# Optimization experiments

Measured on AMD Instinct MI355X. Metric: run time of the kernel, lower is better.

Reference implementation:

```python
import jax, jax.numpy as jnp
import numpy as np

H, D, KV, S, PAST, BS, NB = 32, 128, 8, 128, 8064, 128, 128
T = PAST + S          # total context = 8192
NBLK = T // BS        # logical blocks used = 64
NEG = jnp.float32(-1e30)


def setup_inputs() -> dict:
    key = jax.random.key(0)
    ks = jax.random.split(key, 6)
    q = jax.random.normal(ks[0], (1, H, S, D), jnp.float32)
    k = jax.random.normal(ks[1], (1, KV, S, D), jnp.float32)
    v = jax.random.normal(ks[2], (1, KV, S, D), jnp.float32)
    pk = jax.random.normal(ks[3], (NB, KV, BS, D), jnp.float32)
    pv = jax.random.normal(ks[4], (NB, KV, BS, D), jnp.float32)
    # block table: 64 logical blocks mapped to distinct physical blocks (paged indirection)
    bt = jax.random.permutation(ks[5], NB)[:NBLK].astype(jnp.int32)
    return dict(
        query_state=q, key_state=k, value_state=v,
        attn_mask=jnp.ones((1,), jnp.float32),  # unused: causal prefill path (use_attention_mask=False)
        past_key_state=pk, past_value_state=pv,
        seq_position=PAST,
        scale=jnp.float32(1.0 / np.sqrt(D)),
        block_tables=bt, block_size=BS,
    )


def reference(query_state, key_state, value_state, attn_mask,
              past_key_state, past_value_state, seq_position, scale,
              block_tables, block_size):
    # phase == 'prefill', use_attention_mask=False -> paged_causal_attn_prefill
    kvh = past_key_state.shape[1]
    s_new = query_state.shape[2]
    total = seq_position + s_new  # static python int

    # --- append new K/V into the paged cache at positions [seq_position, total) ---
    pos_new = seq_position + jnp.arange(s_new)
    blk = block_tables[pos_new // block_size]
    off = pos_new % block_size
    k_new = jnp.transpose(key_state[0], (1, 0, 2))    # [S, KV, D]
    v_new = jnp.transpose(value_state[0], (1, 0, 2))
    kc = past_key_state.at[blk, :, off, :].set(k_new)
    vc = past_value_state.at[blk, :, off, :].set(v_new)

    # --- gather the full context [0, total) through the block table ---
    pos = jnp.arange(total)
    blk_a = block_tables[pos // block_size]
    off_a = pos % block_size
    K = kc[blk_a, :, off_a, :]   # [T, KV, D]
    V = vc[blk_a, :, off_a, :]

    # --- grouped-query causal attention ---
    g = query_state.shape[1] // kvh
    q = query_state.reshape(kvh, g, s_new, -1)                 # [KV, G, S, D]
    scores = jnp.einsum('kgsd,tkd->kgst', q, K) * scale        # [KV, G, S, T]
    causal = pos[None, :] <= (seq_position + jnp.arange(s_new))[:, None]  # [S, T]
    scores = jnp.where(causal[None, None], scores, NEG)
    probs = jax.nn.softmax(scores, axis=-1)
    out = jnp.einsum('kgst,tkd->kgsd', probs, V)               # [KV, G, S, D]

    h = kvh * g
    out = out.reshape(1, h, s_new, -1)                         # [1, H, S, D]
    out = jnp.transpose(out, (0, 2, 1, 3)).reshape(1, s_new, h * out.shape[-1])
    return out
```

## Files before the change

### kernel.cpp

```cpp
#include <hip/hip_runtime.h>
#include <hip/hip_bf16.h>


typedef unsigned short u16;
typedef unsigned int u32;
typedef __bf16 bf16x8 __attribute__((ext_vector_type(8)));
typedef float f32x16 __attribute__((ext_vector_type(16)));
typedef float f32x4 __attribute__((ext_vector_type(4)));
typedef u32 u32x4 __attribute__((ext_vector_type(4)));
typedef u32 u32x2 __attribute__((ext_vector_type(2)));
typedef int i32x2 __attribute__((ext_vector_type(2)));

#define NHEAD 32
#define DH 128
#define NKV 8
#define SQ 128
#define PAST_T 8064
#define TOTAL_T 8192
#define BK 64
#define KSTR 136
#define VSTR 66
#define WSPP (16384 + 256)
#define MSUB 17.3123405f

__device__ __forceinline__ u32 pk2f(float lo, float hi) {
  union {
    __hip_bfloat162 b;
    u32 u;
  } cv;
  cv.b = __float22bfloat162_rn(make_float2(lo, hi));
  return cv.u;
}

template <int NPART>
__global__ __launch_bounds__(512, 1) void flash_part(
    const float* __restrict__ q, const float* __restrict__ knew,
    const float* __restrict__ vnew, const float* __restrict__ pk,
    const float* __restrict__ pv, const int* __restrict__ btab,
    const float* __restrict__ scp, float* __restrict__ ws) {
  constexpr int CHUNK = TOTAL_T / NPART;
  constexpr int NITER = CHUNK / BK;
  __shared__ __attribute__((aligned(16))) u16 k_s[2 * BK * KSTR];
  __shared__ __attribute__((aligned(16))) u16 vt_s[2 * DH * VSTR];
  __shared__ int bt_s[64];

  const int bid = blockIdx.x;
  const int kv = bid & 7;
  const int t = bid >> 3;
  const int p = t % NPART;
  const int gp = t / NPART;

  const int tid = threadIdx.x;
  const int wid = tid >> 6;
  const int lane = tid & 63;
  const int g2 = wid & 1;
  const int w = wid >> 1;
  const int h = kv * 4 + gp * 2 + g2;
  const int l31 = lane & 31, grp = lane >> 5;
  const int pstart = p * CHUNK;

  if (tid < 64) bt_s[tid] = btab[tid];
  const float qs = scp[0] * 1.44269504f;

  u32x4 qf[8];
  {
    const float* qp = q + ((size_t)(h * SQ + w * 32 + l31)) * DH;
#pragma unroll
    for (int st = 0; st < 8; ++st) {
      const f32x4 a = *(const f32x4*)(qp + st * 16 + grp * 8);
      const f32x4 b = *(const f32x4*)(qp + st * 16 + grp * 8 + 4);
      u32x4 f;
      f[0] = pk2f(a[0] * qs, a[1] * qs);
      f[1] = pk2f(a[2] * qs, a[3] * qs);
      f[2] = pk2f(b[0] * qs, b[1] * qs);
      f[3] = pk2f(b[2] * qs, b[3] * qs);
      qf[st] = f;
    }
  }

  f32x16 oacc[4];
#pragma unroll
  for (int i = 0; i < 4; ++i)
#pragma unroll
    for (int rr = 0; rr < 16; ++rr) oacc[i][rr] = 0.0f;
  float l_acc = 0.0f;

  __syncthreads();

  f32x4 kr0, kr1, kr2, kr3, v0, v1, v2, v3;
  const int kc4 = (tid & 31) * 4;
  const int ktrow = tid >> 5;
  const int va4 = (tid & 31) * 4;
  const int vtp = tid >> 5;

  auto load_tile = [&](int it) {
    const int t0 = pstart + it * BK;
    const float *sk, *sv;
    if (t0 < PAST_T) {
      const size_t boff =
          (((size_t)bt_s[t0 >> 7] * NKV + kv) * 128 + (t0 & 127)) * (size_t)DH;
      sk = pk + boff;
      sv = pv + boff;
    } else {
      const size_t noff = ((size_t)kv * SQ + (t0 - PAST_T)) * (size_t)DH;
      sk = knew + noff;
      sv = vnew + noff;
    }
    kr0 = *(const f32x4*)(sk + (size_t)(ktrow + 0) * DH + kc4);
    kr1 = *(const f32x4*)(sk + (size_t)(ktrow + 16) * DH + kc4);
    kr2 = *(const f32x4*)(sk + (size_t)(ktrow + 32) * DH + kc4);
    kr3 = *(const f32x4*)(sk + (size_t)(ktrow + 48) * DH + kc4);
    v0 = *(const f32x4*)(sv + (size_t)(2 * vtp) * DH + va4);
    v1 = *(const f32x4*)(sv + (size_t)(2 * vtp + 1) * DH + va4);
    v2 = *(const f32x4*)(sv + (size_t)(2 * vtp + 32) * DH + va4);
    v3 = *(const f32x4*)(sv + (size_t)(2 * vtp + 33) * DH + va4);
  };
  auto store_tile = [&](int buf) {
    u16* ks = k_s + buf * (BK * KSTR);
    u16* vs = vt_s + buf * (DH * VSTR);
    {
      u32x2 pw;
      pw[0] = pk2f(kr0[0], kr0[1]);
      pw[1] = pk2f(kr0[2], kr0[3]);
      *(u32x2*)&ks[(ktrow + 0) * KSTR + kc4] = pw;
    }
    {
      u32x2 pw;
      pw[0] = pk2f(kr1[0], kr1[1]);
      pw[1] = pk2f(kr1[2], kr1[3]);
      *(u32x2*)&ks[(ktrow + 16) * KSTR + kc4] = pw;
    }
    {
      u32x2 pw;
      pw[0] = pk2f(kr2[0], kr2[1]);
      pw[1] = pk2f(kr2[2], kr2[3]);
      *(u32x2*)&ks[(ktrow + 32) * KSTR + kc4] = pw;
    }
    {
      u32x2 pw;
      pw[0] = pk2f(kr3[0], kr3[1]);
      pw[1] = pk2f(kr3[2], kr3[3]);
      *(u32x2*)&ks[(ktrow + 48) * KSTR + kc4] = pw;
    }
#pragma unroll
    for (int j = 0; j < 4; ++j) {
      *(u32*)&vs[(va4 + j) * VSTR + 2 * vtp] = pk2f(v0[j], v1[j]);
      *(u32*)&vs[(va4 + j) * VSTR + 2 * vtp + 32] = pk2f(v2[j], v3[j]);
    }
  };

  load_tile(0);
  store_tile(0);
  __syncthreads();

  for (int it = 0; it < NITER; ++it) {
    const int buf = it & 1;
    if (it + 1 < NITER) load_tile(it + 1);

    const u16* ks = k_s + buf * (BK * KSTR);
    const u16* vs = vt_s + buf * (DH * VSTR);
    const int t0 = pstart + it * BK;
    const int qcol = w * 32 + l31;

    f32x16 sacc0, sacc1;
#pragma unroll
    for (int rr = 0; rr < 16; ++rr) sacc0[rr] = 0.0f;
#pragma unroll
    for (int rr = 0; rr < 16; ++rr) sacc1[rr] = 0.0f;
#pragma unroll
    for (int st = 0; st < 8; ++st) {
      const u32x4 kf0 = *(const u32x4*)&ks[l31 * KSTR + st * 16 + grp * 8];
      sacc0 = __builtin_amdgcn_mfma_f32_32x32x16_bf16(
          __builtin_bit_cast(bf16x8, kf0), __builtin_bit_cast(bf16x8, qf[st]),
          sacc0, 0, 0, 0);
      const u32x4 kf1 =
          *(const u32x4*)&ks[(l31 + 32) * KSTR + st * 16 + grp * 8];
      sacc1 = __builtin_amdgcn_mfma_f32_32x32x16_bf16(
          __builtin_bit_cast(bf16x8, kf1), __builtin_bit_cast(bf16x8, qf[st]),
          sacc1, 0, 0, 0);
    }

#pragma unroll
    for (int ts = 0; ts < 2; ++ts) {
      const f32x16& sacc = ts ? sacc1 : sacc0;
      const int tb = t0 + ts * 32;

      float pr[16];
      if (tb > PAST_T - 32) {
#pragma unroll
        for (int rr = 0; rr < 16; ++rr) {
          const int trow = (rr & 3) + 8 * (rr >> 2) + 4 * grp;
          const float e = exp2f(sacc[rr] - MSUB);
          pr[rr] = ((tb + trow - PAST_T) > qcol) ? 0.0f : e;
        }
      } else {
#pragma unroll
        for (int rr = 0; rr < 16; ++rr) pr[rr] = exp2f(sacc[rr] - MSUB);
      }
      float rs = 0.0f;
#pragma unroll
      for (int rr = 0; rr < 16; ++rr) rs += pr[rr];
      l_acc += rs;

      u32 pkk[8];
#pragma unroll
      for (int j = 0; j < 8; ++j) pkk[j] = pk2f(pr[2 * j], pr[2 * j + 1]);

      u32x4 pf1, pf2;
#if __has_builtin(__builtin_amdgcn_permlane32_swap)
      {
        const i32x2 s02 = __builtin_amdgcn_permlane32_swap(
            (int)pkk[0], (int)pkk[2], false, false);
        const i32x2 s13 = __builtin_amdgcn_permlane32_swap(
            (int)pkk[1], (int)pkk[3], false, false);
        const i32x2 s46 = __builtin_amdgcn_permlane32_swap(
            (int)pkk[4], (int)pkk[6], false, false);
        const i32x2 s57 = __builtin_amdgcn_permlane32_swap(
            (int)pkk[5], (int)pkk[7], false, false);
        pf1[0] = (u32)s02[0];
        pf1[1] = (u32)s13[0];
        pf1[2] = (u32)s02[1];
        pf1[3] = (u32)s13[1];
        pf2[0] = (u32)s46[0];
        pf2[1] = (u32)s57[0];
        pf2[2] = (u32)s46[1];
        pf2[3] = (u32)s57[1];
      }
#else
      {
        u32 xch[8];
#pragma unroll
        for (int j = 0; j < 8; ++j)
          xch[j] = (u32)__shfl_xor((int)pkk[j], 32, 64);
        pf1[0] = grp ? xch[2] : pkk[0];
        pf1[1] = grp ? xch[3] : pkk[1];
        pf1[2] = grp ? pkk[2] : xch[0];
        pf1[3] = grp ? pkk[3] : xch[1];
        pf2[0] = grp ? xch[6] : pkk[4];
        pf2[1] = grp ? xch[7] : pkk[5];
        pf2[2] = grp ? pkk[6] : xch[4];
        pf2[3] = grp ? pkk[7] : xch[5];
      }
#endif

#pragma unroll
      for (int dt = 0; dt < 4; ++dt) {
        const int dd = dt * 32 + l31;
        const u16* vp = &vs[dd * VSTR + ts * 32 + grp * 8];
        u32x4 av;
        av[0] = *(const u32*)(vp + 0);
        av[1] = *(const u32*)(vp + 2);
        av[2] = *(const u32*)(vp + 4);
        av[3] = *(const u32*)(vp + 6);
        oacc[dt] = __builtin_amdgcn_mfma_f32_32x32x16_bf16(
            __builtin_bit_cast(bf16x8, av), __builtin_bit_cast(bf16x8, pf1),
            oacc[dt], 0, 0, 0);
        const u16* vq = vp + 16;
        u32x4 bv;
        bv[0] = *(const u32*)(vq + 0);
        bv[1] = *(const u32*)(vq + 2);
        bv[2] = *(const u32*)(vq + 4);
        bv[3] = *(const u32*)(vq + 6);
        oacc[dt] = __builtin_amdgcn_mfma_f32_32x32x16_bf16(
            __builtin_bit_cast(bf16x8, bv), __builtin_bit_cast(bf16x8, pf2),
            oacc[dt], 0, 0, 0);
      }
    }

    if (it + 1 < NITER) store_tile(buf ^ 1);
    __syncthreads();
  }

  float* wsp = ws + (size_t)(h * NPART + p) * WSPP;
#pragma unroll
  for (int dt = 0; dt < 4; ++dt)
#pragma unroll
    for (int rr = 0; rr < 16; ++rr) {
      const int dd = dt * 32 + (rr & 3) + 8 * (rr >> 2) + 4 * grp;
      wsp[dd * 128 + w * 32 + l31] = oacc[dt][rr];
    }
  const float l_tot = l_acc + __shfl_xor(l_acc, 32, 64);
  if (grp == 0) wsp[16384 + w * 32 + l31] = l_tot;
}

template <int NPART>
__global__ __launch_bounds__(256, 2) void combine_out(
    const float* __restrict__ ws, float* __restrict__ out) {
  __shared__ float rden_s[128];
  __shared__ float tr_s[128 * 9];

  const int dblk = blockIdx.x;
  const int h = blockIdx.y;
  const int tid = threadIdx.x;
  const float* base = ws + (size_t)h * NPART * WSPP;

  if (tid < 128) {
    float denom = 0.0f;
#pragma unroll
    for (int pp = 0; pp < NPART; ++pp)
      denom += base[(size_t)pp * WSPP + 16384 + tid];
    rden_s[tid] = 1.0f / denom;
  }
  __syncthreads();

  const int sq = tid & 31, dr = tid >> 5;
  {
    const int d = dblk * 8 + dr;
    float a[4] = {0.0f, 0.0f, 0.0f, 0.0f};
#pragma unroll
    for (int pp = 0; pp < NPART; ++pp) {
      const f32x4 o = *(const f32x4*)&base[(size_t)pp * WSPP + d * 128 + sq * 4];
#pragma unroll
      for (int j = 0; j < 4; ++j) a[j] += o[j];
    }
#pragma unroll
    for (int j = 0; j < 4; ++j)
      tr_s[(sq * 4 + j) * 9 + dr] = a[j] * rden_s[sq * 4 + j];
  }
  __syncthreads();

  {
    const int s = tid >> 1, dl0 = (tid & 1) * 4;
    f32x4 o;
#pragma unroll
    for (int j = 0; j < 4; ++j) o[j] = tr_s[s * 9 + dl0 + j];
    *(f32x4*)(out + (size_t)s * (NHEAD * DH) + h * DH + dblk * 8 + dl0) = o;
  }
}

extern "C" void kernel_launch(void* const* d_in, const int* in_sizes, int n_in,
                              void* d_out, int out_size, void* d_ws,
                              size_t ws_size, hipStream_t stream) {
  const float* q = (const float*)d_in[0];
  const float* knew = (const float*)d_in[1];
  const float* vnew = (const float*)d_in[2];
  const float* pk = (const float*)d_in[4];
  const float* pv = (const float*)d_in[5];
  const float* scp = (const float*)d_in[7];
  const int* btab = (const int*)d_in[8];
  float* ws = (float*)d_ws;
  float* out = (float*)d_out;

  const size_t need16 = (size_t)NHEAD * 16 * WSPP * sizeof(float);
  const size_t need8 = (size_t)NHEAD * 8 * WSPP * sizeof(float);
  if (ws_size >= need16) {
    flash_part<16><<<dim3(8 * 2 * 16), 512, 0, stream>>>(q, knew, vnew, pk, pv,
                                                         btab, scp, ws);
    combine_out<16><<<dim3(16, NHEAD), 256, 0, stream>>>(ws, out);
  } else if (ws_size >= need8) {
    flash_part<8><<<dim3(8 * 2 * 8), 512, 0, stream>>>(q, knew, vnew, pk, pv,
                                                       btab, scp, ws);
    combine_out<8><<<dim3(16, NHEAD), 256, 0, stream>>>(ws, out);
  }
}
```

Measured before the change: 170.2 us.

## Pre-swizzle V tile into MFMA fragment layout and simplify combine kernel

V tiles are now loaded as scalar columns per thread and stored to shared memory already packed in the MFMA operand-fragment order, so the PV inner loop reads each operand with one 128-bit LDS load instead of four 32-bit loads. This trades coalesced vector global loads of V for strided scalar loads (still coalesced across lanes along D). The combine kernel drops its shared-memory transpose and writes float2 outputs directly, using twice as many blocks with fewer columns each.

Measured after the change: 171.2 us. About the same (+0.6%).

```diff
diff --git a/kernel.cpp b/kernel.cpp
--- a/kernel.cpp
+++ b/kernel.cpp
@@ -19,7 +19,7 @@
 #define TOTAL_T 8192
 #define BK 64
 #define KSTR 136
-#define VSTR 66
+#define VT_SZ 8192
 #define WSPP (16384 + 256)
 #define MSUB 17.3123405f
 
@@ -41,7 +41,7 @@
   constexpr int CHUNK = TOTAL_T / NPART;
   constexpr int NITER = CHUNK / BK;
   __shared__ __attribute__((aligned(16))) u16 k_s[2 * BK * KSTR];
-  __shared__ __attribute__((aligned(16))) u16 vt_s[2 * DH * VSTR];
+  __shared__ __attribute__((aligned(16))) u16 vt_s[2 * VT_SZ];
   __shared__ int bt_s[64];
 
   const int bid = blockIdx.x;
@@ -87,11 +87,17 @@
 
   __syncthreads();
 
-  f32x4 kr0, kr1, kr2, kr3, v0, v1, v2, v3;
+  f32x4 kr0, kr1, kr2, kr3;
+  float va[8], vb[8];
   const int kc4 = (tid & 31) * 4;
   const int ktrow = tid >> 5;
-  const int va4 = (tid & 31) * 4;
-  const int vtp = tid >> 5;
+  const int vd = tid & 127;
+  const int tb8a = tid >> 7;
+  const int vofA =
+      ((((vd >> 5) * 4 + (tb8a >> 1)) * 2 + (tb8a & 1)) * 32 + (vd & 31)) * 8;
+  const int vofB =
+      ((((vd >> 5) * 4 + ((tb8a + 4) >> 1)) * 2 + ((tb8a + 4) & 1)) * 32 +
+       (vd & 31)) * 8;
 
   auto load_tile = [&](int it) {
     const int t0 = pstart + it * BK;
@@ -110,14 +116,16 @@
     kr1 = *(const f32x4*)(sk + (size_t)(ktrow + 16) * DH + kc4);
     kr2 = *(const f32x4*)(sk + (size_t)(ktrow + 32) * DH + kc4);
     kr3 = *(const f32x4*)(sk + (size_t)(ktrow + 48) * DH + kc4);
-    v0 = *(const f32x4*)(sv + (size_t)(2 * vtp) * DH + va4);
-    v1 = *(const f32x4*)(sv + (size_t)(2 * vtp + 1) * DH + va4);
-    v2 = *(const f32x4*)(sv + (size_t)(2 * vtp + 32) * DH + va4);
-    v3 = *(const f32x4*)(sv + (size_t)(2 * vtp + 33) * DH + va4);
+#pragma unroll
+    for (int j = 0; j < 8; ++j)
+      va[j] = sv[(size_t)(tb8a * 8 + j) * DH + vd];
+#pragma unroll
+    for (int j = 0; j < 8; ++j)
+      vb[j] = sv[(size_t)((tb8a + 4) * 8 + j) * DH + vd];
   };
   auto store_tile = [&](int buf) {
     u16* ks = k_s + buf * (BK * KSTR);
-    u16* vs = vt_s + buf * (DH * VSTR);
+    u16* vs = vt_s + buf * VT_SZ;
     {
       u32x2 pw;
       pw[0] = pk2f(kr0[0], kr0[1]);
@@ -142,10 +150,17 @@
       pw[1] = pk2f(kr3[2], kr3[3]);
       *(u32x2*)&ks[(ktrow + 48) * KSTR + kc4] = pw;
     }
-#pragma unroll
-    for (int j = 0; j < 4; ++j) {
-      *(u32*)&vs[(va4 + j) * VSTR + 2 * vtp] = pk2f(v0[j], v1[j]);
-      *(u32*)&vs[(va4 + j) * VSTR + 2 * vtp + 32] = pk2f(v2[j], v3[j]);
+    {
+      u32x4 wa;
+#pragma unroll
+      for (int jj = 0; jj < 4; ++jj) wa[jj] = pk2f(va[2 * jj], va[2 * jj + 1]);
+      *(u32x4*)&vs[vofA] = wa;
+    }
+    {
+      u32x4 wb;
+#pragma unroll
+      for (int jj = 0; jj < 4; ++jj) wb[jj] = pk2f(vb[2 * jj], vb[2 * jj + 1]);
+      *(u32x4*)&vs[vofB] = wb;
     }
   };
 
@@ -158,7 +173,7 @@
     if (it + 1 < NITER) load_tile(it + 1);
 
     const u16* ks = k_s + buf * (BK * KSTR);
-    const u16* vs = vt_s + buf * (DH * VSTR);
+    const u16* vs = vt_s + buf * VT_SZ;
     const int t0 = pstart + it * BK;
     const int qcol = w * 32 + l31;
 
@@ -245,22 +260,14 @@
 
 #pragma unroll
       for (int dt = 0; dt < 4; ++dt) {
-        const int dd = dt * 32 + l31;
-        const u16* vp = &vs[dd * VSTR + ts * 32 + grp * 8];
-        u32x4 av;
-        av[0] = *(const u32*)(vp + 0);
-        av[1] = *(const u32*)(vp + 2);
-        av[2] = *(const u32*)(vp + 4);
-        av[3] = *(const u32*)(vp + 6);
+        const u32x4 av =
+            *(const u32x4*)&vs[((((dt * 4 + ts * 2) * 2 + grp) * 32 + l31)) * 8];
         oacc[dt] = __builtin_amdgcn_mfma_f32_32x32x16_bf16(
             __builtin_bit_cast(bf16x8, av), __builtin_bit_cast(bf16x8, pf1),
             oacc[dt], 0, 0, 0);
-        const u16* vq = vp + 16;
-        u32x4 bv;
-        bv[0] = *(const u32*)(vq + 0);
-        bv[1] = *(const u32*)(vq + 2);
-        bv[2] = *(const u32*)(vq + 4);
-        bv[3] = *(const u32*)(vq + 6);
+        const u32x4 bv =
+            *(const u32x4*)&vs[((((dt * 4 + ts * 2 + 1) * 2 + grp) * 32 + l31)) *
+                               8];
         oacc[dt] = __builtin_amdgcn_mfma_f32_32x32x16_bf16(
             __builtin_bit_cast(bf16x8, bv), __builtin_bit_cast(bf16x8, pf2),
             oacc[dt], 0, 0, 0);
@@ -287,7 +294,6 @@
 __global__ __launch_bounds__(256, 2) void combine_out(
     const float* __restrict__ ws, float* __restrict__ out) {
   __shared__ float rden_s[128];
-  __shared__ float tr_s[128 * 9];
 
   const int dblk = blockIdx.x;
   const int h = blockIdx.y;
@@ -303,29 +309,22 @@
   }
   __syncthreads();
 
-  const int sq = tid & 31, dr = tid >> 5;
-  {
-    const int d = dblk * 8 + dr;
-    float a[4] = {0.0f, 0.0f, 0.0f, 0.0f};
-#pragma unroll
-    for (int pp = 0; pp < NPART; ++pp) {
-      const f32x4 o = *(const f32x4*)&base[(size_t)pp * WSPP + d * 128 + sq * 4];
-#pragma unroll
-      for (int j = 0; j < 4; ++j) a[j] += o[j];
-    }
-#pragma unroll
-    for (int j = 0; j < 4; ++j)
-      tr_s[(sq * 4 + j) * 9 + dr] = a[j] * rden_s[sq * 4 + j];
-  }
-  __syncthreads();
-
-  {
-    const int s = tid >> 1, dl0 = (tid & 1) * 4;
-    f32x4 o;
-#pragma unroll
-    for (int j = 0; j < 4; ++j) o[j] = tr_s[s * 9 + dl0 + j];
-    *(f32x4*)(out + (size_t)s * (NHEAD * DH) + h * DH + dblk * 8 + dl0) = o;
-  }
+  const int qq = tid & 127;
+  const int dp = tid >> 7;
+  const int d0 = dblk * 4 + dp * 2;
+
+  float a0 = 0.0f, a1 = 0.0f;
+#pragma unroll
+  for (int pp = 0; pp < NPART; ++pp) {
+    const float* b = base + (size_t)pp * WSPP;
+    a0 += b[d0 * 128 + qq];
+    a1 += b[(d0 + 1) * 128 + qq];
+  }
+  const float r = rden_s[qq];
+  float2 o;
+  o.x = a0 * r;
+  o.y = a1 * r;
+  *(float2*)(out + (size_t)qq * (NHEAD * DH) + h * DH + d0) = o;
 }
 
 extern "C" void kernel_launch(void* const* d_in, const int* in_sizes, int n_in,
@@ -346,10 +345,10 @@
   if (ws_size >= need16) {
     flash_part<16><<<dim3(8 * 2 * 16), 512, 0, stream>>>(q, knew, vnew, pk, pv,
                                                          btab, scp, ws);
-    combine_out<16><<<dim3(16, NHEAD), 256, 0, stream>>>(ws, out);
+    combine_out<16><<<dim3(32, NHEAD), 256, 0, stream>>>(ws, out);
   } else if (ws_size >= need8) {
     flash_part<8><<<dim3(8 * 2 * 8), 512, 0, stream>>>(q, knew, vnew, pk, pv,
                                                        btab, scp, ws);
-    combine_out<8><<<dim3(16, NHEAD), 256, 0, stream>>>(ws, out);
+    combine_out<8><<<dim3(32, NHEAD), 256, 0, stream>>>(ws, out);
   }
 }
```
